# Optimization experiments

Hardware: AMD Instinct MI355X
Metric: run time of the kernel (lower is better)

## Reference

```python
import jax, jax.numpy as jnp
import numpy as np

N_NODES = 50000
N_EDGES = 800000
D = 64
E_DIM = 2
C = 8


def _spline_basis(pseudo, K):
    """Open B-spline basis, degree=1. pseudo: [Ne, E] in [0,1).
    Returns basis B [Ne, S] and flat weight index WI [Ne, S], S = 2**E."""
    E = pseudo.shape[1]
    v = pseudo * (K - 1)
    lo_f = jnp.floor(v)
    frac = v - lo_f
    lo = lo_f.astype(jnp.int32)
    idx = jnp.stack([jnp.clip(lo, 0, K - 1), jnp.clip(lo + 1, 0, K - 1)], axis=-1)  # [Ne,E,2]
    bas = jnp.stack([1.0 - frac, frac], axis=-1)                                   # [Ne,E,2]
    combos = jnp.asarray(
        np.stack(np.meshgrid(*([np.arange(2)] * E), indexing='ij'), -1).reshape(-1, E)
    )  # [S,E]
    d_idx = jnp.arange(E)[None, :]          # broadcast to [S,E]
    B = jnp.prod(bas[:, d_idx, combos], axis=-1)  # [Ne,S]
    stride = (K ** jnp.arange(E)).astype(jnp.int32)  # [E]
    WI = jnp.sum(idx[:, d_idx, combos] * stride[None, None, :], axis=-1)  # [Ne,S]
    return B, WI


def _spline_conv(x, src, dst, pseudo, W, root, bias, K, num_nodes):
    """SplineConv (degree=1, open spline, aggr='mean', root_weight, bias).
    x: [N,Din], W: [K**E, Din, Dout], root: [Din, Dout]."""
    B, WI = _spline_basis(pseudo, K)                 # [Ne,S], [Ne,S]
    Y = jnp.einsum('nd,kdo->nko', x, W)              # [N, K**E, Dout]
    gathered = Y[src[:, None], WI]                   # [Ne, S, Dout]
    m = jnp.einsum('es,eso->eo', B, gathered)        # [Ne, Dout]
    msum = jax.ops.segment_sum(m, dst, num_segments=num_nodes)
    cnt = jax.ops.segment_sum(jnp.ones((m.shape[0], 1), m.dtype), dst, num_segments=num_nodes)
    aggr = msum / jnp.maximum(cnt, 1.0)
    return aggr + x @ root + bias


def setup_inputs() -> dict:
    key = jax.random.key(0)
    ks = jax.random.split(key, 16)
    s = 1.0 / np.sqrt(D)
    return {
        'x': jax.random.normal(ks[0], (N_NODES, D), jnp.float32),
        'edge_index': jax.random.randint(ks[1], (2, N_EDGES), 0, N_NODES, jnp.int32),
        'edge_attr': jax.random.uniform(ks[2], (N_EDGES, E_DIM), jnp.float32),
        'W1': jax.random.normal(ks[3], (3 ** E_DIM, D, D), jnp.float32) * s,
        'root1': jax.random.normal(ks[4], (D, D), jnp.float32) * s,
        'b1': jax.random.normal(ks[5], (D,), jnp.float32) * 0.01,
        'W2': jax.random.normal(ks[6], (5 ** E_DIM, D, D), jnp.float32) * s,
        'root2': jax.random.normal(ks[7], (D, D), jnp.float32) * s,
        'b2': jax.random.normal(ks[8], (D,), jnp.float32) * 0.01,
        'mlp1_w': jax.random.normal(ks[9], (D, D), jnp.float32) * s,
        'mlp1_b': jax.random.normal(ks[10], (D,), jnp.float32) * 0.01,
        'mlp2_w': jax.random.normal(ks[11], (D, C), jnp.float32) * s,
        'mlp2_b': jax.random.normal(ks[12], (C,), jnp.float32) * 0.01,
    }


def reference(x, edge_index, edge_attr, W1, root1, b1, W2, root2, b2,
              mlp1_w, mlp1_b, mlp2_w, mlp2_b):
    N = x.shape[0]
    src, dst = edge_index[0], edge_index[1]
    h = jax.nn.elu(_spline_conv(x, src, dst, edge_attr, W1, root1, b1, 3, N))
    # dropout is identity in eval mode
    h = jax.nn.elu(_spline_conv(h, src, dst, edge_attr, W2, root2, b2, 5, N))
    # task='node', G=0 -> no pooling / no concat
    h = jax.nn.relu(h @ mlp1_w + mlp1_b)
    h = jax.nn.relu(h @ mlp2_w + mlp2_b)
    return h
```

## Files before the change

kernel.cpp:

```cpp
#include <hip/hip_runtime.h>
#include <hip/hip_fp16.h>

typedef __attribute__((ext_vector_type(8))) short short8;
typedef __attribute__((ext_vector_type(4))) short short4v;
typedef __attribute__((ext_vector_type(4))) unsigned int uint4v;
typedef __attribute__((ext_vector_type(4))) float floatx4;
typedef __attribute__((ext_vector_type(16))) float floatx16;
typedef __fp16 fp16x2_raw __attribute__((ext_vector_type(2)));
typedef _Float16 h2 __attribute__((ext_vector_type(2)));
typedef _Float16 half8 __attribute__((ext_vector_type(8)));

__device__ __forceinline__ unsigned short f2h(float x) {
  _Float16 h = (_Float16)x;
  return __builtin_bit_cast(unsigned short, h);
}
__device__ __forceinline__ float h2f(unsigned short u) {
  return (float)__builtin_bit_cast(_Float16, u);
}

__device__ __forceinline__ void pack_b_dev(
    const float* __restrict__ W, const float* __restrict__ root,
    unsigned short* __restrict__ Bpk, int K2, int i) {
  int j = i & 7;
  int lane = (i >> 3) & 63;
  int rest = i >> 9;
  int wv = rest & 3, kc = rest >> 2;
  int o = wv * 16 + (lane & 15);
  int p = kc * 32 + ((lane >> 4) & 3) * 8 + j;
  int k = p >> 6, q6 = p & 63;
  float v = (k < K2) ? W[(k << 12) + (q6 << 6) + o] : root[(q6 << 6) + o];
  Bpk[i] = f2h(v);
}

__global__ __launch_bounds__(256) void prep_kernel(
    const float* __restrict__ W1, const float* __restrict__ root1,
    unsigned short* __restrict__ Bpk1,
    const float* __restrict__ W2, const float* __restrict__ root2,
    unsigned short* __restrict__ Bpk2,
    const float* __restrict__ m1w, unsigned short* __restrict__ m1pk,
    const float4* __restrict__ X, unsigned short* __restrict__ Xhf,
    int* __restrict__ deg, int N) {
  int nbZ = (N + 255) >> 8;
  int b = blockIdx.x, t = threadIdx.x;
  if (b < nbZ) {
    int i = b * 256 + t;
    if (i < N) deg[i] = 0;
    return;
  }
  b -= nbZ;
  if (b < 160) {
    pack_b_dev(W1, root1, Bpk1, 9, b * 256 + t);
    return;
  }
  b -= 160;
  if (b < 416) {
    pack_b_dev(W2, root2, Bpk2, 25, b * 256 + t);
    return;
  }
  b -= 416;
  if (b < 16) {
    pack_b_dev(m1w, m1w, m1pk, 0, b * 256 + t);
    return;
  }
  b -= 16;
  {
    int i = b * 256 + t;
    if (i < N * 16) {
      float4 v = X[i];
      short4v o = {(short)f2h(v.x), (short)f2h(v.y),
                   (short)f2h(v.z), (short)f2h(v.w)};
      *(short4v*)&Xhf[i * 4] = o;
    }
  }
}

__global__ __launch_bounds__(256) void hist_kernel(
    const int* __restrict__ dst, int* __restrict__ deg, int nE) {
  int e = blockIdx.x * 256 + threadIdx.x;
  if (e < nE) atomicAdd(&deg[dst[e]], 1);
}

__global__ __launch_bounds__(256) void blocksum_kernel(
    const int* __restrict__ deg, int* __restrict__ partial, int N) {
  __shared__ int s[256];
  int t = threadIdx.x, i = blockIdx.x * 256 + t;
  s[t] = (i < N) ? deg[i] : 0;
  __syncthreads();
  for (int off = 128; off > 0; off >>= 1) {
    if (t < off) s[t] += s[t + off];
    __syncthreads();
  }
  if (t == 0) partial[blockIdx.x] = s[0];
}

__global__ __launch_bounds__(256) void blockscan_kernel(
    const int* __restrict__ deg, const int* __restrict__ partial,
    int* __restrict__ row_start, int* __restrict__ cursor,
    int N, int nE, int nb) {
  __shared__ int sp[256];
  __shared__ int s[256];
  __shared__ int base;
  int t = threadIdx.x, i = blockIdx.x * 256 + t;
  int pv = (t < nb) ? partial[t] : 0;
  sp[t] = pv;
  __syncthreads();
  for (int off = 1; off < 256; off <<= 1) {
    int x = (t >= off) ? sp[t - off] : 0;
    __syncthreads();
    sp[t] += x;
    __syncthreads();
  }
  if (t == blockIdx.x) base = sp[t] - pv;
  __syncthreads();
  int v = (i < N) ? deg[i] : 0;
  s[t] = v;
  __syncthreads();
  for (int off = 1; off < 256; off <<= 1) {
    int x = (t >= off) ? s[t - off] : 0;
    __syncthreads();
    s[t] += x;
    __syncthreads();
  }
  if (i < N) {
    int excl = s[t] - v + base;
    row_start[i] = excl;
    cursor[i] = excl;
  }
  if (i == 0) row_start[N] = nE;
}

__global__ __launch_bounds__(256) void scatter_rec_kernel(
    const int* __restrict__ dst, const int* __restrict__ src,
    const float* __restrict__ attr, int* __restrict__ cursor,
    float4* __restrict__ recS, int nE) {
  int e = blockIdx.x * 256 + threadIdx.x;
  if (e < 32) recS[nE + e] = make_float4(0.f, 0.f, 0.f, 0.f);
  if (e >= nE) return;
  int pos = atomicAdd(&cursor[dst[e]], 1);
  float2 a = *(const float2*)&attr[2 * e];
  recS[pos] = make_float4(a.x * 4.f, a.y * 4.f,
                          __builtin_bit_cast(float, src[e] * 64), 0.f);
}

template <int K, int K2, int OUTF16, int NODES, int GRP, int MINW, int PF, int HEAD>
__global__ __launch_bounds__(256, MINW) void spline_layer_kernel(
    const float4* __restrict__ rec, const int* __restrict__ row_start,
    const unsigned short* __restrict__ Xhf, const unsigned short* __restrict__ Bpk,
    const float* __restrict__ bias, void* __restrict__ outv, int N, float uscale,
    const unsigned short* __restrict__ m1pk_g, const float* __restrict__ m1b_g,
    const float* __restrict__ m2w_g, const float* __restrict__ m2b_g) {
  constexpr int RZ = K2 * 64;
  constexpr int AS = RZ + 8;
  constexpr int NKZ = RZ / 32;
  constexpr int NKC = (K2 + 1) * 2;
  __shared__ unsigned short As[NODES * AS];
  __shared__ __align__(16) float invs[16];
  __shared__ int wcur;
  const int t = threadIdx.x, w = t >> 6, lane = t & 63;
  const int nodeBase = blockIdx.x * NODES;

  const int col = lane & 31, half = lane >> 5, col2 = col * 2;
  const float mi0f = (col < K2) ? (float)(col % K) : -1e9f;
  const float mi1f = (col < K2) ? (float)(col / K) : 0.f;
  const h2 nus2 = {(_Float16)(-uscale), (_Float16)(-uscale)};
  const h2 m0s2 = {(_Float16)mi0f, (_Float16)mi0f};
  const h2 m1s2 = {(_Float16)mi1f, (_Float16)mi1f};
  const h2 one2 = {(_Float16)1.f, (_Float16)1.f};
  const h2 zer2 = {(_Float16)0.f, (_Float16)0.f};

  if (t == 0) wcur = 0;
  if constexpr (NODES < 16) {
    if (w == 3 && lane >= 48 + NODES) invs[lane - 48] = 1.0f;
  }
  __syncthreads();

  int row;
  if (lane == 0) row = atomicAdd(&wcur, 1);
  row = __shfl(row, 0);
  while (row < NODES) {
    const int node = nodeBase + row;
    if (node < N) {
      floatx16 d0, d1;
#pragma unroll
      for (int i = 0; i < 16; ++i) { d0[i] = 0.f; d1[i] = 0.f; }

      const int beg = row_start[node], end = row_start[node + 1];
      if (lane == 0) invs[row] = 1.f / (float)max(end - beg, 1);

      float4 rjn[8];
      if constexpr (PF) {
        const int ib0 = beg + half * 8;
#pragma unroll
        for (int j = 0; j < 8; ++j) rjn[j] = rec[ib0 + j];
      }
      for (int c0 = beg; c0 < end; c0 += 16) {
        float4 rj[8];
        if constexpr (PF) {
#pragma unroll
          for (int j = 0; j < 8; ++j) rj[j] = rjn[j];
        } else {
          const int ib = c0 + half * 8;
#pragma unroll
          for (int j = 0; j < 8; ++j) rj[j] = rec[ib + j];
        }
        unsigned int xv[8];
#pragma unroll
        for (int j = 0; j < 8; ++j)
          xv[j] = *(const unsigned int*)(Xhf +
                    (__builtin_bit_cast(int, rj[j].z) + col2));
        if constexpr (PF) {
          const int ibn = c0 + 16 + half * 8;
#pragma unroll
          for (int j = 0; j < 8; ++j) rjn[j] = rec[ibn + j];
        }
        const bool fullc = (end - c0 >= 16);
        const int rem = end - (c0 + half * 8);
        unsigned int aw[4];
#pragma unroll
        for (int i = 0; i < 4; ++i) {
          fp16x2_raw uxr =
              __builtin_amdgcn_cvt_pkrtz(rj[2 * i].x, rj[2 * i + 1].x);
          fp16x2_raw uyr =
              __builtin_amdgcn_cvt_pkrtz(rj[2 * i].y, rj[2 * i + 1].y);
          h2 ux = __builtin_bit_cast(h2, uxr);
          h2 uy = __builtin_bit_cast(h2, uyr);
          h2 t0 = ux * nus2 + m0s2;
          h2 t1 = uy * nus2 + m1s2;
          h2 s0 = __builtin_elementwise_max(
                      one2 - __builtin_elementwise_abs(t0), zer2);
          h2 s1 = __builtin_elementwise_max(
                      one2 - __builtin_elementwise_abs(t1), zer2);
          h2 p = s0 * s1;
          unsigned int pw = __builtin_bit_cast(unsigned int, p);
          if (!fullc) {
            if (2 * i >= rem) pw = 0;
            else if (2 * i + 1 >= rem) pw &= 0xFFFFu;
          }
          aw[i] = pw;
        }
        uint4v Awv = {aw[0], aw[1], aw[2], aw[3]};
        half8 A = __builtin_bit_cast(half8, Awv);
        uint4v blo, bhi;
#pragma unroll
        for (int i = 0; i < 4; ++i) {
          blo[i] = __builtin_amdgcn_perm(xv[2 * i + 1], xv[2 * i], 0x05040100u);
          bhi[i] = __builtin_amdgcn_perm(xv[2 * i + 1], xv[2 * i], 0x07060302u);
        }
        d0 = __builtin_amdgcn_mfma_f32_32x32x16_f16(
                 A, __builtin_bit_cast(half8, blo), d0, 0, 0, 0);
        d1 = __builtin_amdgcn_mfma_f32_32x32x16_f16(
                 A, __builtin_bit_cast(half8, bhi), d1, 0, 0, 0);
      }

#pragma unroll
      for (int reg = 0; reg < 16; ++reg) {
        int r = (reg & 3) + 8 * (reg >> 2) + 4 * half;
        if (r < K2) {
          fp16x2_raw z = __builtin_amdgcn_cvt_pkrtz(d0[reg], d1[reg]);
          *(unsigned int*)&As[row * AS + r * 64 + col2] =
              __builtin_bit_cast(unsigned int, z);
        }
      }
    } else {
      if (lane == 0) invs[row] = 1.0f;
      for (int i = lane; i < RZ / 2; i += 64)
        ((unsigned int*)&As[row * AS])[i] = 0;
    }
    if (lane == 0) row = atomicAdd(&wcur, 1);
    row = __shfl(row, 0);
  }
  __syncthreads();

  const int mrow = lane & 15, q = lane >> 4;
  const int arow = (NODES < 16) ? min(mrow, NODES - 1) : mrow;
  const int anode = min(nodeBase + arow, N - 1);
  floatx4 aZ0 = {0.f, 0.f, 0.f, 0.f};
  floatx4 aZ1 = {0.f, 0.f, 0.f, 0.f};
  floatx4 aR  = {0.f, 0.f, 0.f, 0.f};
#pragma unroll
  for (int kc0 = 0; kc0 < NKC; kc0 += GRP) {
    short8 av[GRP], bv[GRP];
#pragma unroll
    for (int u = 0; u < GRP; ++u) {
      const int kc = kc0 + u;
      if (kc < NKZ)
        av[u] = *(const short8*)&As[arow * AS + kc * 32 + q * 8];
      else
        av[u] = *(const short8*)&Xhf[(size_t)anode * 64 + (kc - NKZ) * 32 + q * 8];
      bv[u] = *(const short8*)&Bpk[(((size_t)kc * 4 + w) * 64 + lane) * 8];
    }
#pragma unroll
    for (int u = 0; u < GRP; ++u) {
      const int kc = kc0 + u;
      if (kc >= NKZ)
        aR = __builtin_amdgcn_mfma_f32_16x16x32_f16(
                 __builtin_bit_cast(half8, av[u]),
                 __builtin_bit_cast(half8, bv[u]), aR, 0, 0, 0);
      else if ((kc0 / GRP) & 1)
        aZ1 = __builtin_amdgcn_mfma_f32_16x16x32_f16(
                  __builtin_bit_cast(half8, av[u]),
                  __builtin_bit_cast(half8, bv[u]), aZ1, 0, 0, 0);
      else
        aZ0 = __builtin_amdgcn_mfma_f32_16x16x32_f16(
                  __builtin_bit_cast(half8, av[u]),
                  __builtin_bit_cast(half8, bv[u]), aZ0, 0, 0, 0);
    }
  }

  const int o = w * 16 + mrow;
  const float bvs = bias[o];
  const floatx4 invv = *(const floatx4*)&invs[q * 4];

  if constexpr (HEAD) {
    __syncthreads();
    unsigned short* Hs = As;
    unsigned short* Ts = As + 2048;
    float* W2s = (float*)(As + 4096);
    for (int i = t; i < 512; i += 256) W2s[i] = m2w_g[i];
#pragma unroll
    for (int reg = 0; reg < 4; ++reg) {
      int rloc = q * 4 + reg;
      int node = nodeBase + rloc;
      if (rloc < NODES && node < N) {
        float v = (aZ0[reg] + aZ1[reg]) * invv[reg] + aR[reg] + bvs;
        v = v > 0.f ? v : (expf(v) - 1.f);
        Hs[rloc * 72 + o] = f2h(v);
      }
    }
    __syncthreads();
    floatx4 accT = {0.f, 0.f, 0.f, 0.f};
#pragma unroll
    for (int kc = 0; kc < 2; ++kc) {
      short8 a = *(const short8*)&Hs[arow * 72 + kc * 32 + q * 8];
      short8 b = *(const short8*)&m1pk_g[(((size_t)kc * 4 + w) * 64 + lane) * 8];
      accT = __builtin_amdgcn_mfma_f32_16x16x32_f16(
                 __builtin_bit_cast(half8, a),
                 __builtin_bit_cast(half8, b), accT, 0, 0, 0);
    }
    const float bT = m1b_g[o];
#pragma unroll
    for (int reg = 0; reg < 4; ++reg) {
      float v = accT[reg] + bT;
      Ts[(q * 4 + reg) * 72 + o] = f2h(v > 0.f ? v : 0.f);
    }
    __syncthreads();
    if (t < NODES * 8) {
      int nl = t >> 3, c = t & 7;
      int node = nodeBase + nl;
      if (node < N) {
        float s = m2b_g[c];
        for (int d = 0; d < 64; ++d) s += h2f(Ts[nl * 72 + d]) * W2s[d * 8 + c];
        ((float*)outv)[(size_t)node * 8 + c] = s > 0.f ? s : 0.f;
      }
    }
  } else {
#pragma unroll
    for (int reg = 0; reg < 4; ++reg) {
      int rloc = q * 4 + reg;
      int node = nodeBase + rloc;
      if (rloc < NODES && node < N) {
        float v = (aZ0[reg] + aZ1[reg]) * invv[reg] + aR[reg] + bvs;
        v = v > 0.f ? v : (expf(v) - 1.f);
        if (OUTF16)
          ((unsigned short*)outv)[(size_t)node * 64 + o] = f2h(v);
        else
          ((float*)outv)[(size_t)node * 64 + o] = v;
      }
    }
  }
}

extern "C" void kernel_launch(void* const* d_in, const int* in_sizes, int n_in,
                              void* d_out, int out_size, void* d_ws, size_t ws_size,
                              hipStream_t stream) {
  const float* x     = (const float*)d_in[0];
  const int*   ei    = (const int*)d_in[1];
  const float* attr  = (const float*)d_in[2];
  const float* W1    = (const float*)d_in[3];
  const float* root1 = (const float*)d_in[4];
  const float* b1    = (const float*)d_in[5];
  const float* W2    = (const float*)d_in[6];
  const float* root2 = (const float*)d_in[7];
  const float* b2    = (const float*)d_in[8];
  const float* m1w   = (const float*)d_in[9];
  const float* m1b   = (const float*)d_in[10];
  const float* m2w   = (const float*)d_in[11];
  const float* m2b   = (const float*)d_in[12];

  const int N  = in_sizes[0] / 64;
  const int nE = in_sizes[1] / 2;
  const int* src  = ei;
  const int* dstv = ei + nE;
  float* out = (float*)d_out;

  int* deg       = (int*)d_ws;
  int* row_start = deg + N;
  int* cursor    = row_start + (N + 1);
  int* partial   = cursor + N;
  char* pbase = (char*)(partial + 256);
  pbase = (char*)(((uintptr_t)pbase + 15) & ~(uintptr_t)15);
  float4* recS = (float4*)pbase;
  unsigned short* Xhf  = (unsigned short*)(recS + nE + 32);
  unsigned short* h1hf = Xhf + (size_t)N * 64;
  unsigned short* Bpk1 = h1hf + (size_t)N * 64;
  unsigned short* Bpk2 = Bpk1 + 64 * 640;
  unsigned short* m1pk = Bpk2 + 64 * 1664;

  dim3 blk(256);
  int nbN  = (N + 255) / 256;
  int nbE  = (nE + 255) / 256;
  int nbF1 = (N + 15) / 16;
  int nbF2 = (N + 11) / 12;
  int nbP  = nbN + 160 + 416 + 16 + (N * 16 + 255) / 256;

  prep_kernel<<<nbP, blk, 0, stream>>>(W1, root1, Bpk1, W2, root2, Bpk2,
                                       m1w, m1pk, (const float4*)x, Xhf,
                                       deg, N);

  hist_kernel<<<nbE, blk, 0, stream>>>(dstv, deg, nE);
  blocksum_kernel<<<nbN, blk, 0, stream>>>(deg, partial, N);
  blockscan_kernel<<<nbN, blk, 0, stream>>>(deg, partial, row_start, cursor,
                                            N, nE, nbN);
  scatter_rec_kernel<<<nbE, blk, 0, stream>>>(dstv, src, attr, cursor, recS, nE);

  spline_layer_kernel<3, 9, 1, 16, 4, 4, 0, 0><<<nbF1, blk, 0, stream>>>(
      recS, row_start, Xhf, Bpk1, b1, h1hf, N, 0.5f,
      m1pk, m1b, m2w, m2b);

  spline_layer_kernel<5, 25, 0, 12, 4, 4, 1, 1><<<nbF2, blk, 0, stream>>>(
      recS, row_start, h1hf, Bpk2, b2, out, N, 1.0f,
      m1pk, m1b, m2w, m2b);
}
```

Baseline: 298.4 us.

## Compact edge records to 8 bytes and deepen prefetch pipeline in spline layer

Edge records shrink from a float4 (16 bytes) to a uint2 holding the two pseudo-coordinates packed as fp16 plus the pre-scaled source offset. This halves the record traffic in both the scatter and the spline aggregation kernels. The prefetch path now also issues the X-row gathers and computes the basis one chunk ahead of the MFMA step, so gather latency overlaps with compute. The costs are more live registers, which may lower occupancy, and fp16 rounding of the pseudo-coordinates happening earlier than before.

Result: no change. 298.8 us (+0.1%).

```diff
diff --git a/kernel.cpp b/kernel.cpp
--- a/kernel.cpp
+++ b/kernel.cpp
@@ -132,19 +132,20 @@
 __global__ __launch_bounds__(256) void scatter_rec_kernel(
     const int* __restrict__ dst, const int* __restrict__ src,
     const float* __restrict__ attr, int* __restrict__ cursor,
-    float4* __restrict__ recS, int nE) {
+    uint2* __restrict__ recS, int nE) {
   int e = blockIdx.x * 256 + threadIdx.x;
-  if (e < 32) recS[nE + e] = make_float4(0.f, 0.f, 0.f, 0.f);
+  if (e < 48) recS[nE + e] = make_uint2(0u, 0u);
   if (e >= nE) return;
   int pos = atomicAdd(&cursor[dst[e]], 1);
   float2 a = *(const float2*)&attr[2 * e];
-  recS[pos] = make_float4(a.x * 4.f, a.y * 4.f,
-                          __builtin_bit_cast(float, src[e] * 64), 0.f);
+  fp16x2_raw uv = __builtin_amdgcn_cvt_pkrtz(a.x * 4.f, a.y * 4.f);
+  recS[pos] = make_uint2(__builtin_bit_cast(unsigned int, uv),
+                         (unsigned int)(src[e] * 64));
 }
 
 template <int K, int K2, int OUTF16, int NODES, int GRP, int MINW, int PF, int HEAD>
 __global__ __launch_bounds__(256, MINW) void spline_layer_kernel(
-    const float4* __restrict__ rec, const int* __restrict__ row_start,
+    const uint2* __restrict__ rec, const int* __restrict__ row_start,
     const unsigned short* __restrict__ Xhf, const unsigned short* __restrict__ Bpk,
     const float* __restrict__ bias, void* __restrict__ outv, int N, float uscale,
     const unsigned short* __restrict__ m1pk_g, const float* __restrict__ m1b_g,
@@ -187,45 +188,18 @@
       const int beg = row_start[node], end = row_start[node + 1];
       if (lane == 0) invs[row] = 1.f / (float)max(end - beg, 1);
 
-      float4 rjn[8];
-      if constexpr (PF) {
-        const int ib0 = beg + half * 8;
-#pragma unroll
-        for (int j = 0; j < 8; ++j) rjn[j] = rec[ib0 + j];
-      }
-      for (int c0 = beg; c0 < end; c0 += 16) {
-        float4 rj[8];
-        if constexpr (PF) {
-#pragma unroll
-          for (int j = 0; j < 8; ++j) rj[j] = rjn[j];
-        } else {
-          const int ib = c0 + half * 8;
-#pragma unroll
-          for (int j = 0; j < 8; ++j) rj[j] = rec[ib + j];
-        }
-        unsigned int xv[8];
-#pragma unroll
-        for (int j = 0; j < 8; ++j)
-          xv[j] = *(const unsigned int*)(Xhf +
-                    (__builtin_bit_cast(int, rj[j].z) + col2));
-        if constexpr (PF) {
-          const int ibn = c0 + 16 + half * 8;
-#pragma unroll
-          for (int j = 0; j < 8; ++j) rjn[j] = rec[ibn + j];
-        }
-        const bool fullc = (end - c0 >= 16);
-        const int rem = end - (c0 + half * 8);
+      auto basis = [&](const uint2* rr, int cc0) -> half8 {
+        const bool fullc = (end - cc0 >= 16);
+        const int rem = end - (cc0 + half * 8);
         unsigned int aw[4];
 #pragma unroll
         for (int i = 0; i < 4; ++i) {
-          fp16x2_raw uxr =
-              __builtin_amdgcn_cvt_pkrtz(rj[2 * i].x, rj[2 * i + 1].x);
-          fp16x2_raw uyr =
-              __builtin_amdgcn_cvt_pkrtz(rj[2 * i].y, rj[2 * i + 1].y);
-          h2 ux = __builtin_bit_cast(h2, uxr);
-          h2 uy = __builtin_bit_cast(h2, uyr);
-          h2 t0 = ux * nus2 + m0s2;
-          h2 t1 = uy * nus2 + m1s2;
+          unsigned int ux = __builtin_amdgcn_perm(rr[2 * i + 1].x, rr[2 * i].x,
+                                                  0x05040100u);
+          unsigned int uy = __builtin_amdgcn_perm(rr[2 * i + 1].x, rr[2 * i].x,
+                                                  0x07060302u);
+          h2 t0 = __builtin_bit_cast(h2, ux) * nus2 + m0s2;
+          h2 t1 = __builtin_bit_cast(h2, uy) * nus2 + m1s2;
           h2 s0 = __builtin_elementwise_max(
                       one2 - __builtin_elementwise_abs(t0), zer2);
           h2 s1 = __builtin_elementwise_max(
@@ -239,17 +213,60 @@
           aw[i] = pw;
         }
         uint4v Awv = {aw[0], aw[1], aw[2], aw[3]};
-        half8 A = __builtin_bit_cast(half8, Awv);
+        return __builtin_bit_cast(half8, Awv);
+      };
+      auto mfma_step = [&](half8 A, const unsigned int* xvp,
+                           floatx16& dd0, floatx16& dd1) {
         uint4v blo, bhi;
 #pragma unroll
         for (int i = 0; i < 4; ++i) {
-          blo[i] = __builtin_amdgcn_perm(xv[2 * i + 1], xv[2 * i], 0x05040100u);
-          bhi[i] = __builtin_amdgcn_perm(xv[2 * i + 1], xv[2 * i], 0x07060302u);
+          blo[i] = __builtin_amdgcn_perm(xvp[2 * i + 1], xvp[2 * i], 0x05040100u);
+          bhi[i] = __builtin_amdgcn_perm(xvp[2 * i + 1], xvp[2 * i], 0x07060302u);
         }
-        d0 = __builtin_amdgcn_mfma_f32_32x32x16_f16(
-                 A, __builtin_bit_cast(half8, blo), d0, 0, 0, 0);
-        d1 = __builtin_amdgcn_mfma_f32_32x32x16_f16(
-                 A, __builtin_bit_cast(half8, bhi), d1, 0, 0, 0);
+        dd0 = __builtin_amdgcn_mfma_f32_32x32x16_f16(
+                  A, __builtin_bit_cast(half8, blo), dd0, 0, 0, 0);
+        dd1 = __builtin_amdgcn_mfma_f32_32x32x16_f16(
+                  A, __builtin_bit_cast(half8, bhi), dd1, 0, 0, 0);
+      };
+
+      if constexpr (PF) {
+        const int ibh = beg + half * 8;
+        uint2 rjn[8];
+        unsigned int xv[8], xvn[8];
+        half8 A, An;
+#pragma unroll
+        for (int j = 0; j < 8; ++j) rjn[j] = rec[ibh + j];
+#pragma unroll
+        for (int j = 0; j < 8; ++j)
+          xv[j] = *(const unsigned int*)(Xhf + (int)rjn[j].y + col2);
+        A = basis(rjn, beg);
+#pragma unroll
+        for (int j = 0; j < 8; ++j) rjn[j] = rec[ibh + 16 + j];
+        for (int c0 = beg; c0 < end; c0 += 16) {
+#pragma unroll
+          for (int j = 0; j < 8; ++j)
+            xvn[j] = *(const unsigned int*)(Xhf + (int)rjn[j].y + col2);
+          An = basis(rjn, c0 + 16);
+#pragma unroll
+          for (int j = 0; j < 8; ++j) rjn[j] = rec[c0 + 32 + half * 8 + j];
+          mfma_step(A, xv, d0, d1);
+          A = An;
+#pragma unroll
+          for (int j = 0; j < 8; ++j) xv[j] = xvn[j];
+        }
+      } else {
+        for (int c0 = beg; c0 < end; c0 += 16) {
+          const int ib = c0 + half * 8;
+          uint2 rj[8];
+#pragma unroll
+          for (int j = 0; j < 8; ++j) rj[j] = rec[ib + j];
+          unsigned int xv[8];
+#pragma unroll
+          for (int j = 0; j < 8; ++j)
+            xv[j] = *(const unsigned int*)(Xhf + (int)rj[j].y + col2);
+          half8 A = basis(rj, c0);
+          mfma_step(A, xv, d0, d1);
+        }
       }
 
 #pragma unroll
@@ -399,8 +416,8 @@
   int* partial   = cursor + N;
   char* pbase = (char*)(partial + 256);
   pbase = (char*)(((uintptr_t)pbase + 15) & ~(uintptr_t)15);
-  float4* recS = (float4*)pbase;
-  unsigned short* Xhf  = (unsigned short*)(recS + nE + 32);
+  uint2* recS = (uint2*)pbase;
+  unsigned short* Xhf  = (unsigned short*)(recS + nE + 48);
   unsigned short* h1hf = Xhf + (size_t)N * 64;
   unsigned short* Bpk1 = h1hf + (size_t)N * 64;
   unsigned short* Bpk2 = Bpk1 + 64 * 640;
```

## Pack edge records to 8 bytes with fp16 attrs and stage row_start in LDS

Applied to the files above, without the earlier changes.

Edge records shrink from a 16-byte float4 to an 8-byte uint2. The scaled pseudo-coordinates are packed as fp16x2 when the record is scattered, so the layer kernels unpack them with a byte perm and no longer convert per chunk. This halves record traffic in the scatter and in both spline layers, and the block's row_start values are now loaded once into shared memory. In exchange the pseudo-coordinates are rounded to fp16 earlier, though the older path converted them to fp16 anyway.

Result: faster. 282.3 us, median of 2 (-5.4%).

```diff
diff --git a/kernel.cpp b/kernel.cpp
--- a/kernel.cpp
+++ b/kernel.cpp
@@ -132,19 +132,20 @@
 __global__ __launch_bounds__(256) void scatter_rec_kernel(
     const int* __restrict__ dst, const int* __restrict__ src,
     const float* __restrict__ attr, int* __restrict__ cursor,
-    float4* __restrict__ recS, int nE) {
+    uint2* __restrict__ recS, int nE) {
   int e = blockIdx.x * 256 + threadIdx.x;
-  if (e < 32) recS[nE + e] = make_float4(0.f, 0.f, 0.f, 0.f);
+  if (e < 32) recS[nE + e] = make_uint2(0u, 0u);
   if (e >= nE) return;
   int pos = atomicAdd(&cursor[dst[e]], 1);
   float2 a = *(const float2*)&attr[2 * e];
-  recS[pos] = make_float4(a.x * 4.f, a.y * 4.f,
-                          __builtin_bit_cast(float, src[e] * 64), 0.f);
+  fp16x2_raw uv = __builtin_amdgcn_cvt_pkrtz(a.x * 4.f, a.y * 4.f);
+  recS[pos] = make_uint2(__builtin_bit_cast(unsigned int, uv),
+                         (unsigned int)(src[e] * 64));
 }
 
 template <int K, int K2, int OUTF16, int NODES, int GRP, int MINW, int PF, int HEAD>
 __global__ __launch_bounds__(256, MINW) void spline_layer_kernel(
-    const float4* __restrict__ rec, const int* __restrict__ row_start,
+    const uint2* __restrict__ rec, const int* __restrict__ row_start,
     const unsigned short* __restrict__ Xhf, const unsigned short* __restrict__ Bpk,
     const float* __restrict__ bias, void* __restrict__ outv, int N, float uscale,
     const unsigned short* __restrict__ m1pk_g, const float* __restrict__ m1b_g,
@@ -155,6 +156,7 @@
   constexpr int NKC = (K2 + 1) * 2;
   __shared__ unsigned short As[NODES * AS];
   __shared__ __align__(16) float invs[16];
+  __shared__ int rs[17];
   __shared__ int wcur;
   const int t = threadIdx.x, w = t >> 6, lane = t & 63;
   const int nodeBase = blockIdx.x * NODES;
@@ -169,6 +171,10 @@
   const h2 zer2 = {(_Float16)0.f, (_Float16)0.f};
 
   if (t == 0) wcur = 0;
+  if (t <= NODES) {
+    int idx = min(nodeBase + t, N);
+    rs[t] = row_start[idx];
+  }
   if constexpr (NODES < 16) {
     if (w == 3 && lane >= 48 + NODES) invs[lane - 48] = 1.0f;
   }
@@ -184,48 +190,21 @@
 #pragma unroll
       for (int i = 0; i < 16; ++i) { d0[i] = 0.f; d1[i] = 0.f; }
 
-      const int beg = row_start[node], end = row_start[node + 1];
+      const int beg = rs[row], end = rs[row + 1];
       if (lane == 0) invs[row] = 1.f / (float)max(end - beg, 1);
 
-      float4 rjn[8];
-      if constexpr (PF) {
-        const int ib0 = beg + half * 8;
-#pragma unroll
-        for (int j = 0; j < 8; ++j) rjn[j] = rec[ib0 + j];
-      }
-      for (int c0 = beg; c0 < end; c0 += 16) {
-        float4 rj[8];
-        if constexpr (PF) {
-#pragma unroll
-          for (int j = 0; j < 8; ++j) rj[j] = rjn[j];
-        } else {
-          const int ib = c0 + half * 8;
-#pragma unroll
-          for (int j = 0; j < 8; ++j) rj[j] = rec[ib + j];
-        }
-        unsigned int xv[8];
-#pragma unroll
-        for (int j = 0; j < 8; ++j)
-          xv[j] = *(const unsigned int*)(Xhf +
-                    (__builtin_bit_cast(int, rj[j].z) + col2));
-        if constexpr (PF) {
-          const int ibn = c0 + 16 + half * 8;
-#pragma unroll
-          for (int j = 0; j < 8; ++j) rjn[j] = rec[ibn + j];
-        }
-        const bool fullc = (end - c0 >= 16);
-        const int rem = end - (c0 + half * 8);
+      auto basis = [&](const uint2* rr, int cc0) -> half8 {
+        const bool fullc = (end - cc0 >= 16);
+        const int rem = end - (cc0 + half * 8);
         unsigned int aw[4];
 #pragma unroll
         for (int i = 0; i < 4; ++i) {
-          fp16x2_raw uxr =
-              __builtin_amdgcn_cvt_pkrtz(rj[2 * i].x, rj[2 * i + 1].x);
-          fp16x2_raw uyr =
-              __builtin_amdgcn_cvt_pkrtz(rj[2 * i].y, rj[2 * i + 1].y);
-          h2 ux = __builtin_bit_cast(h2, uxr);
-          h2 uy = __builtin_bit_cast(h2, uyr);
-          h2 t0 = ux * nus2 + m0s2;
-          h2 t1 = uy * nus2 + m1s2;
+          unsigned int ux = __builtin_amdgcn_perm(rr[2 * i + 1].x, rr[2 * i].x,
+                                                  0x05040100u);
+          unsigned int uy = __builtin_amdgcn_perm(rr[2 * i + 1].x, rr[2 * i].x,
+                                                  0x07060302u);
+          h2 t0 = __builtin_bit_cast(h2, ux) * nus2 + m0s2;
+          h2 t1 = __builtin_bit_cast(h2, uy) * nus2 + m1s2;
           h2 s0 = __builtin_elementwise_max(
                       one2 - __builtin_elementwise_abs(t0), zer2);
           h2 s1 = __builtin_elementwise_max(
@@ -239,7 +218,35 @@
           aw[i] = pw;
         }
         uint4v Awv = {aw[0], aw[1], aw[2], aw[3]};
-        half8 A = __builtin_bit_cast(half8, Awv);
+        return __builtin_bit_cast(half8, Awv);
+      };
+
+      uint2 rjn[8];
+      if constexpr (PF) {
+        const int ib0 = beg + half * 8;
+#pragma unroll
+        for (int j = 0; j < 8; ++j) rjn[j] = rec[ib0 + j];
+      }
+      for (int c0 = beg; c0 < end; c0 += 16) {
+        uint2 rj[8];
+        if constexpr (PF) {
+#pragma unroll
+          for (int j = 0; j < 8; ++j) rj[j] = rjn[j];
+        } else {
+          const int ib = c0 + half * 8;
+#pragma unroll
+          for (int j = 0; j < 8; ++j) rj[j] = rec[ib + j];
+        }
+        unsigned int xv[8];
+#pragma unroll
+        for (int j = 0; j < 8; ++j)
+          xv[j] = *(const unsigned int*)(Xhf + (int)rj[j].y + col2);
+        if constexpr (PF) {
+          const int ibn = c0 + 16 + half * 8;
+#pragma unroll
+          for (int j = 0; j < 8; ++j) rjn[j] = rec[ibn + j];
+        }
+        half8 A = basis(rj, c0);
         uint4v blo, bhi;
 #pragma unroll
         for (int i = 0; i < 4; ++i) {
@@ -399,7 +406,7 @@
   int* partial   = cursor + N;
   char* pbase = (char*)(partial + 256);
   pbase = (char*)(((uintptr_t)pbase + 15) & ~(uintptr_t)15);
-  float4* recS = (float4*)pbase;
+  uint2* recS = (uint2*)pbase;
   unsigned short* Xhf  = (unsigned short*)(recS + nE + 32);
   unsigned short* h1hf = Xhf + (size_t)N * 64;
   unsigned short* Bpk1 = h1hf + (size_t)N * 64;
```
